# Kernel tuning notes

Hardware: AMD Instinct MI355X
Metric: run time of the kernel (lower is better)

The kernel has to match this reference:

```python
import jax, jax.numpy as jnp
import numpy as np

N, S, W, H = 256, 64, 256, 32   # node_num, sensor_num, slide_win, gru_hid_size
ALPHA = 0.2
NEG = -9e15


def gat(h, adj, Wm, a):
    """pyGAT GraphAttentionLayer (concat=False, dropout=0 / eval).
    h: [..., M, din], adj: [..., M, M], Wm: [..., din, dout], a: [..., 2*dout]."""
    Wh = jnp.einsum('...mi,...io->...mo', h, Wm)
    dout = Wm.shape[-1]
    f1 = jnp.einsum('...mo,...o->...m', Wh, a[..., :dout])
    f2 = jnp.einsum('...mo,...o->...m', Wh, a[..., dout:])
    e = jax.nn.leaky_relu(f1[..., :, None] + f2[..., None, :], negative_slope=ALPHA)
    att = jax.nn.softmax(jnp.where(adj > 0, e, NEG), axis=-1)
    return jnp.einsum('...mk,...ko->...mo', att, Wh)


def gru_cell(h, x, Wih, Whh, bih, bhh):
    # per-node batched torch GRU cell; gate order r, z, n
    gi = jnp.einsum('ngi,ni->ng', Wih, x) + bih
    gh = jnp.einsum('ngh,nh->ng', Whh, h) + bhh
    ir, iz, inn = jnp.split(gi, 3, axis=-1)
    hr, hz, hn = jnp.split(gh, 3, axis=-1)
    r = jax.nn.sigmoid(ir + hr)
    z = jax.nn.sigmoid(iz + hz)
    n = jnp.tanh(inn + r * hn)
    return (1.0 - z) * n + z * h


def gru2(xseq, h0, Wih0, Whh0, bih0, bhh0, Wih1, Whh1, bih1, bhh1):
    # xseq: [N, S, Din] (seq axis = sensor axis), h0: [2, N, H] -> ([N,S,H], [2,N,H])
    def step(carry, x_t):
        h0c, h1c = carry
        h0n = gru_cell(h0c, x_t, Wih0, Whh0, bih0, bhh0)
        h1n = gru_cell(h1c, h0n, Wih1, Whh1, bih1, bhh1)
        return (h0n, h1n), h1n
    (h0f, h1f), ys = jax.lax.scan(step, (h0[0], h0[1]), jnp.swapaxes(xseq, 0, 1))
    return jnp.swapaxes(ys, 0, 1), jnp.stack([h0f, h1f])


def setup_inputs():
    key = jax.random.key(0)
    ks = jax.random.split(key, 32)
    def rn(k, shape, scale=0.05):
        return jax.random.normal(k, shape, dtype=jnp.float32) * scale
    inp = {}
    inp['x'] = jax.random.normal(ks[0], (N, S, W), dtype=jnp.float32)
    inp['Feature_adj_sub'] = jax.random.randint(ks[1], (N, S, S), 0, 2).astype(jnp.float32)
    inp['Time_adj_sub'] = jax.random.randint(ks[2], (N, W, W), 0, 2).astype(jnp.float32)
    inp['adj'] = jax.random.randint(ks[3], (N, N), 0, 2).astype(jnp.float32)
    inp['H_pre'] = jax.random.normal(ks[4], (2, N, H), dtype=jnp.float32)
    # per-node GAT params (stacked over nodes)
    inp['Fatt_W'] = rn(ks[5], (N, W, W)); inp['Fatt_a'] = rn(ks[6], (N, 2 * W))
    inp['Tatt_W'] = rn(ks[7], (N, S, S)); inp['Tatt_a'] = rn(ks[8], (N, 2 * S))
    # per-node 2-layer GRU params
    inp['Wih0'] = rn(ks[9], (N, 3 * H, 3 * W)); inp['Whh0'] = rn(ks[10], (N, 3 * H, H))
    inp['bih0'] = rn(ks[11], (N, 3 * H)); inp['bhh0'] = rn(ks[12], (N, 3 * H))
    inp['Wih1'] = rn(ks[13], (N, 3 * H, H)); inp['Whh1'] = rn(ks[14], (N, 3 * H, H))
    inp['bih1'] = rn(ks[15], (N, 3 * H)); inp['bhh1'] = rn(ks[16], (N, 3 * H))
    # per-node 3-layer FC
    inp['fc1_w'] = rn(ks[17], (N, H, H)); inp['fc1_b'] = rn(ks[18], (N, H))
    inp['fc2_w'] = rn(ks[19], (N, H, H)); inp['fc2_b'] = rn(ks[20], (N, H))
    inp['fc3_w'] = rn(ks[21], (N, 1, H)); inp['fc3_b'] = rn(ks[22], (N, 1))
    # global output GATs
    inp['oW'] = rn(ks[23], (S, S)); inp['oa'] = rn(ks[24], (2 * S,))
    inp['o1W'] = rn(ks[25], (S, S)); inp['o1a'] = rn(ks[26], (2 * S,))
    inp['o2W'] = rn(ks[27], (2 * S, S)); inp['o2a'] = rn(ks[28], (2 * S,))
    return inp


def reference(x, Feature_adj_sub, Time_adj_sub, adj, H_pre,
              Fatt_W, Fatt_a, Tatt_W, Tatt_a,
              Wih0, Whh0, bih0, bhh0, Wih1, Whh1, bih1, bhh1,
              fc1_w, fc1_b, fc2_w, fc2_b, fc3_w, fc3_b,
              oW, oa, o1W, o1a, o2W, o2a):
    # batched over all nodes at once (replaces Python loop over node_num)
    Fat = gat(x, Feature_adj_sub, Fatt_W, Fatt_a)                    # [N,S,W]
    Tat = gat(jnp.swapaxes(x, 1, 2), Time_adj_sub, Tatt_W, Tatt_a)   # [N,W,S]
    cat_at = jnp.concatenate([Fat, jnp.swapaxes(Tat, 1, 2), x], axis=-1)  # [N,S,3W]
    gru_out, cat_H = gru2(cat_at, H_pre, Wih0, Whh0, bih0, bhh0,
                          Wih1, Whh1, bih1, bhh1)                    # [N,S,H],[2,N,H]
    h = jax.nn.relu(jnp.einsum('nsh,nkh->nsk', gru_out, fc1_w) + fc1_b[:, None, :])
    h = jax.nn.relu(jnp.einsum('nsh,nkh->nsk', h, fc2_w) + fc2_b[:, None, :])
    ct = (jnp.einsum('nsh,nkh->nsk', h, fc3_w) + fc3_b[:, None, :])[..., 0]  # [N,S]
    out = gat(ct, adj, oW, oa)
    out1 = gat(ct, adj, o1W, o1a)
    finalout = gat(jnp.concatenate([out, out1], axis=-1), adj, o2W, o2a)
    return finalout, cat_H
```

## Files before the change

kernel.cpp:

```cpp
#include <hip/hip_runtime.h>
#include <hip/hip_bf16.h>

__device__ __forceinline__ float sigf(float x){ return __builtin_amdgcn_rcpf(1.f+__expf(-x)); }
__device__ __forceinline__ float tanhfa(float x){
  return 1.f - 2.f*__builtin_amdgcn_rcpf(1.f + __expf(2.f*x));
}

#define ALPHA 0.2f
#define NEGV  -9e15f


__device__ __forceinline__ void gl2lds16(const float* g, float* l){
  __builtin_amdgcn_global_load_lds(
      (const __attribute__((address_space(1))) void*)g,
      (__attribute__((address_space(3))) void*)l, 16, 0, 0);
}

__global__ __launch_bounds__(256) void k_mask(const float* __restrict__ src,
                                              unsigned* __restrict__ dst, int nelem){
  const int stride = gridDim.x * blockDim.x;
  const int lane = threadIdx.x & 63;
  for (int e = blockIdx.x*blockDim.x + threadIdx.x; e < nelem; e += stride){
    unsigned long long m = __ballot(src[e] > 0.f);
    if (lane == 0)       dst[e >> 5] = (unsigned)m;
    else if (lane == 32) dst[e >> 5] = (unsigned)(m >> 32);
  }
}

__global__ __launch_bounds__(256) void k3_wht(const float* __restrict__ x,
                                              const float* __restrict__ TW,
                                              const float* __restrict__ Ta,
                                              float* __restrict__ WhTt,
                                              float* __restrict__ Tf1p,
                                              float* __restrict__ Tf2p){
  const int n = blockIdx.x >> 1, ch = blockIdx.x & 1, c0 = ch*32;
  const int tid = threadIdx.x;
  __shared__ float Wm[64][36];
  __shared__ float as1[32], as2[32];
  for (int idx = tid; idx < 2048; idx += 256){
    int k = idx >> 5, cc = idx & 31;
    Wm[k][cc] = TW[n*4096 + k*64 + c0 + cc];
  }
  if (tid < 32){ as1[tid] = Ta[n*128 + c0 + tid]; as2[tid] = Ta[n*128 + 64 + c0 + tid]; }
  __syncthreads();
  const int i = tid;
  const float* xn = x + n*16384;
  float acc[32];
#pragma unroll
  for (int c = 0; c < 32; ++c) acc[c] = 0.f;
#pragma unroll 2
  for (int k = 0; k < 64; ++k){
    float xv = xn[k*256 + i];
    const float* wr = &Wm[k][0];
#pragma unroll
    for (int c = 0; c < 32; ++c) acc[c] = fmaf(xv, wr[c], acc[c]);
  }
  float f1 = 0.f, f2 = 0.f;
#pragma unroll
  for (int c = 0; c < 32; ++c){ f1 = fmaf(acc[c], as1[c], f1); f2 = fmaf(acc[c], as2[c], f2); }
  Tf1p[ch*65536 + n*256 + i] = f1;
  Tf2p[ch*65536 + n*256 + i] = f2;
  float* o = WhTt + n*16384;
#pragma unroll
  for (int c = 0; c < 32; ++c) o[(c0+c)*256 + i] = acc[c];
}

__global__ __launch_bounds__(256) void k4_tat(const float* __restrict__ WhTt,
                                              const float* __restrict__ Tf1p,
                                              const float* __restrict__ Tf2p,
                                              const unsigned* __restrict__ maskT,
                                              float* __restrict__ TatT){
  const int n = blockIdx.x >> 1, ch = blockIdx.x & 1, c0 = ch*32;
  const int i = threadIdx.x;
  __shared__ float f2s[256];
  __shared__ float wt[64][36];
  const float f1 = Tf1p[n*256 + i] + Tf1p[65536 + n*256 + i];
  f2s[i] = Tf2p[n*256 + i] + Tf2p[65536 + n*256 + i];
  unsigned mw[8];
#pragma unroll
  for (int w = 0; w < 8; ++w) mw[w] = maskT[n*2048 + i*8 + w];
  __syncthreads();
  float m = -INFINITY;
  for (int w = 0; w < 8; ++w){
    const unsigned mk = mw[w];
#pragma unroll
    for (int bb = 0; bb < 32; ++bb){
      float e = f1 + f2s[(w<<5)+bb]; e = (e > 0.f) ? e : ALPHA*e;
      e = ((mk >> bb) & 1u) ? e : NEGV;
      m = fmaxf(m, e);
    }
  }
  float s = 0.f;
  for (int w = 0; w < 8; ++w){
    const unsigned mk = mw[w];
#pragma unroll
    for (int bb = 0; bb < 32; ++bb){
      float e = f1 + f2s[(w<<5)+bb]; e = (e > 0.f) ? e : ALPHA*e;
      e = ((mk >> bb) & 1u) ? e : NEGV;
      s += __expf(e - m);
    }
  }
  const float inv = 1.f / s;
  float acc[32];
#pragma unroll
  for (int c = 0; c < 32; ++c) acc[c] = 0.f;
  for (int jt = 0; jt < 4; ++jt){
    __syncthreads();
    for (int idx = i; idx < 2048; idx += 256){
      int cc = idx >> 6, jj = idx & 63;
      wt[jj][cc] = WhTt[n*16384 + (c0+cc)*256 + (jt<<6) + jj];
    }
    __syncthreads();
    for (int jj = 0; jj < 64; ++jj){
      const int j = (jt<<6) + jj;
      float e = f1 + f2s[j]; e = (e > 0.f) ? e : ALPHA*e;
      e = ((mw[j>>5] >> (j & 31)) & 1u) ? e : NEGV;
      const float p = __expf(e - m) * inv;
      const float* wr = &wt[jj][0];
#pragma unroll
      for (int c = 0; c < 32; ++c) acc[c] = fmaf(p, wr[c], acc[c]);
    }
  }
  float* o = TatT + n*16384;
#pragma unroll
  for (int c = 0; c < 32; ++c) o[(c0+c)*256 + i] = acc[c];
}

__global__ __launch_bounds__(256) void k1_whf(const float* __restrict__ x,
                                              const float* __restrict__ FW,
                                              float* __restrict__ WhF){
  const int n = blockIdx.x >> 1, ch = blockIdx.x & 1, c0 = ch*128;
  const int tid = threadIdx.x;
  __shared__ float xt[16384];
  {
    const int w = tid >> 6, l = tid & 63;
    const float* xg = x + n*16384 + w*4096 + l*4;
    float* ld = &xt[w*4096];
#pragma unroll
    for (int j = 0; j < 16; ++j) gl2lds16(xg + j*256, ld + j*256);
  }
  asm volatile("s_waitcnt vmcnt(0)" ::: "memory");
  __syncthreads();
  const int cq = tid & 31, iq = tid >> 5;
  const int cc = c0 + cq*4;
  const float* Wn = FW + (size_t)n*65536 + cc;
  const float* xrow = &xt[iq*8*256];
  float acc[8][4];
#pragma unroll
  for (int i = 0; i < 8; ++i)
#pragma unroll
    for (int c = 0; c < 4; ++c) acc[i][c] = 0.f;
#pragma unroll 2
  for (int k4 = 0; k4 < 64; ++k4){
    const float4 w0 = *(const float4*)&Wn[(4*k4+0)*256];
    const float4 w1 = *(const float4*)&Wn[(4*k4+1)*256];
    const float4 w2 = *(const float4*)&Wn[(4*k4+2)*256];
    const float4 w3 = *(const float4*)&Wn[(4*k4+3)*256];
#pragma unroll
    for (int i = 0; i < 8; ++i){
      const float4 xv = *(const float4*)&xrow[i*256 + 4*k4];
      acc[i][0] = fmaf(xv.x, w0.x, acc[i][0]); acc[i][0] = fmaf(xv.y, w1.x, acc[i][0]);
      acc[i][0] = fmaf(xv.z, w2.x, acc[i][0]); acc[i][0] = fmaf(xv.w, w3.x, acc[i][0]);
      acc[i][1] = fmaf(xv.x, w0.y, acc[i][1]); acc[i][1] = fmaf(xv.y, w1.y, acc[i][1]);
      acc[i][1] = fmaf(xv.z, w2.y, acc[i][1]); acc[i][1] = fmaf(xv.w, w3.y, acc[i][1]);
      acc[i][2] = fmaf(xv.x, w0.z, acc[i][2]); acc[i][2] = fmaf(xv.y, w1.z, acc[i][2]);
      acc[i][2] = fmaf(xv.z, w2.z, acc[i][2]); acc[i][2] = fmaf(xv.w, w3.z, acc[i][2]);
      acc[i][3] = fmaf(xv.x, w0.w, acc[i][3]); acc[i][3] = fmaf(xv.y, w1.w, acc[i][3]);
      acc[i][3] = fmaf(xv.z, w2.w, acc[i][3]); acc[i][3] = fmaf(xv.w, w3.w, acc[i][3]);
    }
  }
  float* o = WhF + n*16384 + cc;
#pragma unroll
  for (int i = 0; i < 8; ++i)
    *(float4*)&o[(iq*8 + i)*256] = make_float4(acc[i][0], acc[i][1], acc[i][2], acc[i][3]);
}

__global__ __launch_bounds__(512) void k2_fat(const float* __restrict__ WhF,
                                              const float* __restrict__ Fa,
                                              const float* __restrict__ Fadj,
                                              float* __restrict__ Fat){
  const int n = blockIdx.x, tid = threadIdx.x;
  __shared__ float attT[64][68];
  __shared__ float f1s[64], f2s[64];
  __shared__ float part[64][8][2];
  const float* Wh = WhF + n*16384;
  {
    int i = tid >> 3, q = tid & 7;
    const float* an = Fa + n*512;
    float p1 = 0.f, p2 = 0.f;
    for (int cc = 0; cc < 32; ++cc){
      int c2 = q*32 + cc;
      float w = Wh[i*256 + c2];
      p1 = fmaf(w, an[c2], p1);
      p2 = fmaf(w, an[256 + c2], p2);
    }
    part[i][q][0] = p1; part[i][q][1] = p2;
  }
  __syncthreads();
  if (tid < 64){
    float s1 = 0.f, s2 = 0.f;
#pragma unroll
    for (int q = 0; q < 8; ++q){ s1 += part[tid][q][0]; s2 += part[tid][q][1]; }
    f1s[tid] = s1; f2s[tid] = s2;
  }
  __syncthreads();
  if (tid < 64){
    const int r = tid;
    const float f1 = f1s[r];
    const float* adjr = Fadj + n*4096 + r*64;
    unsigned m0 = 0, m1 = 0;
#pragma unroll
    for (int j = 0; j < 32; ++j) if (adjr[j] > 0.f) m0 |= (1u << j);
#pragma unroll
    for (int j = 0; j < 32; ++j) if (adjr[32+j] > 0.f) m1 |= (1u << j);
    float m = -INFINITY;
#pragma unroll
    for (int j = 0; j < 64; ++j){
      float e = f1 + f2s[j]; e = (e > 0.f) ? e : ALPHA*e;
      unsigned bit = (j < 32) ? ((m0 >> j) & 1u) : ((m1 >> (j-32)) & 1u);
      e = bit ? e : NEGV;
      m = fmaxf(m, e);
    }
    float s = 0.f;
#pragma unroll
    for (int j = 0; j < 64; ++j){
      float e = f1 + f2s[j]; e = (e > 0.f) ? e : ALPHA*e;
      unsigned bit = (j < 32) ? ((m0 >> j) & 1u) : ((m1 >> (j-32)) & 1u);
      e = bit ? e : NEGV;
      s += __expf(e - m);
    }
    const float inv = 1.f / s;
#pragma unroll
    for (int j = 0; j < 64; ++j){
      float e = f1 + f2s[j]; e = (e > 0.f) ? e : ALPHA*e;
      unsigned bit = (j < 32) ? ((m0 >> j) & 1u) : ((m1 >> (j-32)) & 1u);
      e = bit ? e : NEGV;
      attT[j][r] = __expf(e - m) * inv;
    }
  }
  __syncthreads();
  const int c = tid & 255, ih = tid >> 8;
  float acc[32];
#pragma unroll
  for (int i = 0; i < 32; ++i) acc[i] = 0.f;
#pragma unroll 2
  for (int j = 0; j < 64; ++j){
    float w = Wh[j*256 + c];
    const float* ar = &attT[j][ih*32];
#pragma unroll
    for (int i = 0; i < 32; ++i) acc[i] = fmaf(ar[i], w, acc[i]);
  }
  float* o = Fat + n*16384;
#pragma unroll
  for (int i = 0; i < 32; ++i) o[(ih*32 + i)*256 + c] = acc[i];
}

__global__ __launch_bounds__(256) void k5_gi0(const float* __restrict__ Fat,
                                              const float* __restrict__ TatT,
                                              const float* __restrict__ x,
                                              const float* __restrict__ Wih0,
                                              float* __restrict__ P0,
                                              float* __restrict__ P1,
                                              float* __restrict__ P2){
  const int n = blockIdx.x & 255, s = blockIdx.x >> 8;
  const int tid = threadIdx.x;
  const int l = tid & 63, w = tid >> 6;
  const int a = tid & 31, b = tid >> 5;
  __shared__ float cl[2][2048];
  __shared__ float wl[2][3072];
  const float* src = (s == 0) ? (Fat + n*16384)
                   : (s == 1) ? (TatT + n*16384)
                              : (x + n*16384);
  const float* Wseg = Wih0 + (size_t)n*73728 + s*256;
  const int lr = l >> 3, lc = l & 7, sc = lc ^ lr;
  const float* cg0 = src + (16*w + lr)*256 + sc*4;
  const float* cg1 = cg0 + 8*256;
  const float* wg0 = Wseg + (size_t)(24*w + lr)*768 + lc*4;
  const float* wg1 = wg0 + (size_t)8*768;
  const float* wg2 = wg0 + (size_t)16*768;

#define K5_STAGE(BF, K0) do {                       \
    gl2lds16(cg0 + (K0), &cl[BF][512*w]);           \
    gl2lds16(cg1 + (K0), &cl[BF][512*w + 256]);     \
    gl2lds16(wg0 + (K0), &wl[BF][768*w]);           \
    gl2lds16(wg1 + (K0), &wl[BF][768*w + 256]);     \
    gl2lds16(wg2 + (K0), &wl[BF][768*w + 512]);     \
  } while (0)

  float acc[12][2];
#pragma unroll
  for (int gi = 0; gi < 12; ++gi){ acc[gi][0] = 0.f; acc[gi][1] = 0.f; }

  int bf = 0;
  K5_STAGE(0, 0);
  const int ax4 = (a & 7) << 2;
#pragma unroll 1
  for (int kt = 0; kt < 8; ++kt){
    if (kt < 7){
      K5_STAGE(bf ^ 1, (kt + 1) * 32);
      asm volatile("s_waitcnt vmcnt(5)" ::: "memory");
    } else {
      asm volatile("s_waitcnt vmcnt(0)" ::: "memory");
    }
    __builtin_amdgcn_s_barrier();
    const float* clb  = &cl[bf][a*32];
    const float* clb2 = &cl[bf][(a+32)*32];
    const float* wlb  = &wl[bf][b*384];
#pragma unroll
    for (int k4 = 0; k4 < 8; ++k4){
      const int j4 = (k4 << 2) ^ ax4;
      const float4 c0 = *(const float4*)&clb[j4];
      const float4 c1 = *(const float4*)&clb2[j4];
#pragma unroll
      for (int gi = 0; gi < 12; ++gi){
        const float4 wv = *(const float4*)&wlb[gi*32 + (k4 << 2)];
        float a0 = acc[gi][0], a1 = acc[gi][1];
        a0 = fmaf(wv.x, c0.x, a0); a1 = fmaf(wv.x, c1.x, a1);
        a0 = fmaf(wv.y, c0.y, a0); a1 = fmaf(wv.y, c1.y, a1);
        a0 = fmaf(wv.z, c0.z, a0); a1 = fmaf(wv.z, c1.z, a1);
        a0 = fmaf(wv.w, c0.w, a0); a1 = fmaf(wv.w, c1.w, a1);
        acc[gi][0] = a0; acc[gi][1] = a1;
      }
    }
    __builtin_amdgcn_s_barrier();
    bf ^= 1;
  }
#undef K5_STAGE
  float* o = (s == 0) ? (P0 + n*16384)
           : (s == 1) ? (P1 + n*16384)
                      : (P2 + n*8192);
#pragma unroll
  for (int q = 0; q < 3; ++q){
    *(float4*)&o[a*96 + b*12 + q*4] =
        make_float4(acc[4*q][0], acc[4*q+1][0], acc[4*q+2][0], acc[4*q+3][0]);
    *(float4*)&o[(a+32)*96 + b*12 + q*4] =
        make_float4(acc[4*q][1], acc[4*q+1][1], acc[4*q+2][1], acc[4*q+3][1]);
  }
}

__global__ __launch_bounds__(128) void k6_gru(const float* __restrict__ G0,
                                              const float* __restrict__ G1,
                                              const float* __restrict__ G2,
                                              const float* __restrict__ Hpre,
                                              const float* __restrict__ Whh0,
                                              const float* __restrict__ bih0,
                                              const float* __restrict__ bhh0,
                                              const float* __restrict__ Wih1,
                                              const float* __restrict__ Whh1,
                                              const float* __restrict__ bih1,
                                              const float* __restrict__ bhh1,
                                              const float* __restrict__ fc1w,
                                              const float* __restrict__ fc1b,
                                              const float* __restrict__ fc2w,
                                              const float* __restrict__ fc2b,
                                              const float* __restrict__ fc3w,
                                              const float* __restrict__ fc3b,
                                              float* __restrict__ ct,
                                              float* __restrict__ dout){
  const int n = blockIdx.x, tid = threadIdx.x;
  const int wid = tid >> 6, l = tid & 63;
  const int g2 = l & 31, co = (l >> 5) * 16;
  __shared__ float ginS[6144];
  __shared__ float h0buf[2][32];
  __shared__ float h1buf[2][32];
  __shared__ float hist[64][33];
  __shared__ float Wst[32][33];
  __shared__ float b1s[32], b2s[32], w3s[32];
  {
    const float4* p0 = (const float4*)(G0 + n*16384);
    const float4* p1 = (const float4*)(G1 + n*16384);
    const float4* p2 = (const float4*)(G2 + n*8192);
    float4* gs = (float4*)ginS;
#pragma unroll
    for (int j = 0; j < 12; ++j){
      int idx = j*128 + tid;
      float4 a = p0[idx], b = p1[idx], c = p2[idx];
      gs[idx] = make_float4(a.x+b.x+c.x, a.y+b.y+c.y, a.z+b.z+c.z, a.w+b.w+c.w);
    }
  }
  if (tid < 32){
    b1s[tid] = fc1b[n*32 + tid];
    b2s[tid] = fc2b[n*32 + tid];
    w3s[tid] = fc3w[n*32 + tid];
  }
  for (int idx = tid; idx < 1024; idx += 128) Wst[idx>>5][idx&31] = fc1w[n*1024 + idx];
  float wr_[16], wz_[16], wn_[16];
  float ur_[16], uz_[16], un_[16];
  {
    const float* WA = (wid == 0) ? (Whh0 + n*3072) : (Wih1 + n*3072);
#pragma unroll
    for (int q = 0; q < 4; ++q){
      float4 v;
      v = *(const float4*)(WA + g2*32 + co + 4*q);       wr_[4*q]=v.x; wr_[4*q+1]=v.y; wr_[4*q+2]=v.z; wr_[4*q+3]=v.w;
      v = *(const float4*)(WA + (32+g2)*32 + co + 4*q);  wz_[4*q]=v.x; wz_[4*q+1]=v.y; wz_[4*q+2]=v.z; wz_[4*q+3]=v.w;
      v = *(const float4*)(WA + (64+g2)*32 + co + 4*q);  wn_[4*q]=v.x; wn_[4*q+1]=v.y; wn_[4*q+2]=v.z; wn_[4*q+3]=v.w;
    }
    if (wid == 1){
      const float* WB = Whh1 + n*3072;
#pragma unroll
      for (int q = 0; q < 4; ++q){
        float4 v;
        v = *(const float4*)(WB + g2*32 + co + 4*q);       ur_[4*q]=v.x; ur_[4*q+1]=v.y; ur_[4*q+2]=v.z; ur_[4*q+3]=v.w;
        v = *(const float4*)(WB + (32+g2)*32 + co + 4*q);  uz_[4*q]=v.x; uz_[4*q+1]=v.y; uz_[4*q+2]=v.z; uz_[4*q+3]=v.w;
        v = *(const float4*)(WB + (64+g2)*32 + co + 4*q);  un_[4*q]=v.x; un_[4*q+1]=v.y; un_[4*q+2]=v.z; un_[4*q+3]=v.w;
      }
    }
  }
  const float* bip = (wid == 0) ? bih0 : bih1;
  const float* bhp = (wid == 0) ? bhh0 : bhh1;
  const float br = bip[n*96 + g2], bz = bip[n*96 + 32 + g2], bn = bip[n*96 + 64 + g2];
  const float cr = bhp[n*96 + g2], cz = bhp[n*96 + 32 + g2], cn = bhp[n*96 + 64 + g2];
  const float* hp = (wid == 0) ? (Hpre + n*32) : (Hpre + 8192 + n*32);
  float hown = hp[g2];
  float hs[16];
#pragma unroll
  for (int q = 0; q < 4; ++q){
    float4 v = *(const float4*)&hp[co + 4*q];
    hs[4*q]=v.x; hs[4*q+1]=v.y; hs[4*q+2]=v.z; hs[4*q+3]=v.w;
  }
  for (int s = 0; s < 65; ++s){
    __syncthreads();
    if (wid == 0){
      if (s < 64){
        const float gr = ginS[s*96 + g2], gz = ginS[s*96 + 32 + g2], gn = ginS[s*96 + 64 + g2];
        if (s > 0){
#pragma unroll
          for (int q = 0; q < 4; ++q){
            float4 v = *(const float4*)&h0buf[(s-1)&1][co + 4*q];
            hs[4*q]=v.x; hs[4*q+1]=v.y; hs[4*q+2]=v.z; hs[4*q+3]=v.w;
          }
        }
        float pr = 0.f, pz = 0.f, pn = 0.f;
#pragma unroll
        for (int j = 0; j < 16; ++j){
          pr = fmaf(wr_[j], hs[j], pr);
          pz = fmaf(wz_[j], hs[j], pz);
          pn = fmaf(wn_[j], hs[j], pn);
        }
        pr += __shfl_xor(pr, 32);
        pz += __shfl_xor(pz, 32);
        pn += __shfl_xor(pn, 32);
        const float r = sigf(gr + br + pr + cr);
        const float z = sigf(gz + bz + pz + cz);
        const float nn = tanhfa(gn + bn + r*(pn + cn));
        hown = (1.f - z)*nn + z*hown;
        if (l < 32) h0buf[s & 1][g2] = hown;
      }
    } else {
      if (s >= 1){
        const int t = s - 1;
        if (s > 1){
#pragma unroll
          for (int q = 0; q < 4; ++q){
            float4 v = *(const float4*)&h1buf[(s-1)&1][co + 4*q];
            hs[4*q]=v.x; hs[4*q+1]=v.y; hs[4*q+2]=v.z; hs[4*q+3]=v.w;
          }
        }
        float hx[16];
#pragma unroll
        for (int q = 0; q < 4; ++q){
          float4 v = *(const float4*)&h0buf[(s-1)&1][co + 4*q];
          hx[4*q]=v.x; hx[4*q+1]=v.y; hx[4*q+2]=v.z; hx[4*q+3]=v.w;
        }
        float qr = 0.f, qz = 0.f, qn = 0.f, sr = 0.f, sz = 0.f, sn = 0.f;
#pragma unroll
        for (int j = 0; j < 16; ++j){
          qr = fmaf(wr_[j], hx[j], qr);  sr = fmaf(ur_[j], hs[j], sr);
          qz = fmaf(wz_[j], hx[j], qz);  sz = fmaf(uz_[j], hs[j], sz);
          qn = fmaf(wn_[j], hx[j], qn);  sn = fmaf(un_[j], hs[j], sn);
        }
        float vr = qr + sr; vr += __shfl_xor(vr, 32);
        float vz = qz + sz; vz += __shfl_xor(vz, 32);
        qn += __shfl_xor(qn, 32);
        sn += __shfl_xor(sn, 32);
        const float r1 = sigf(vr + br + cr);
        const float z1 = sigf(vz + bz + cz);
        const float n1 = tanhfa(qn + bn + r1*(sn + cn));
        hown = (1.f - z1)*n1 + z1*hown;
        if (l < 32){ h1buf[s & 1][g2] = hown; hist[t][g2] = hown; }
      }
    }
  }
  if (wid == 0 && l < 32) dout[16384 + n*32 + g2] = hown;
  if (wid == 1 && l < 32) dout[16384 + 8192 + n*32 + g2] = hown;
  __syncthreads();
  float r1a[32];
  if (tid < 64){
    float hr[32];
#pragma unroll
    for (int k = 0; k < 32; ++k) hr[k] = hist[tid][k];
#pragma unroll
    for (int k = 0; k < 32; ++k){
      float a0=0.f,a1=0.f,a2=0.f,a3=0.f;
#pragma unroll
      for (int q = 0; q < 32; q += 4){
        a0 = fmaf(hr[q],   Wst[k][q],   a0);
        a1 = fmaf(hr[q+1], Wst[k][q+1], a1);
        a2 = fmaf(hr[q+2], Wst[k][q+2], a2);
        a3 = fmaf(hr[q+3], Wst[k][q+3], a3);
      }
      float v = b1s[k] + ((a0+a1)+(a2+a3));
      r1a[k] = v > 0.f ? v : 0.f;
    }
  }
  __syncthreads();
  for (int idx = tid; idx < 1024; idx += 128) Wst[idx>>5][idx&31] = fc2w[n*1024 + idx];
  __syncthreads();
  if (tid < 64){
    float r2a[32];
#pragma unroll
    for (int k = 0; k < 32; ++k){
      float a0=0.f,a1=0.f,a2=0.f,a3=0.f;
#pragma unroll
      for (int q = 0; q < 32; q += 4){
        a0 = fmaf(r1a[q],   Wst[k][q],   a0);
        a1 = fmaf(r1a[q+1], Wst[k][q+1], a1);
        a2 = fmaf(r1a[q+2], Wst[k][q+2], a2);
        a3 = fmaf(r1a[q+3], Wst[k][q+3], a3);
      }
      float v = b2s[k] + ((a0+a1)+(a2+a3));
      r2a[k] = v > 0.f ? v : 0.f;
    }
    float v = fc3b[n];
#pragma unroll
    for (int k = 0; k < 32; ++k) v = fmaf(r2a[k], w3s[k], v);
    ct[n*64 + tid] = v;
  }
}

__global__ __launch_bounds__(256) void k8a(const float* __restrict__ ct,
                                           const float* __restrict__ W0,
                                           const float* __restrict__ a0,
                                           const float* __restrict__ W1,
                                           const float* __restrict__ a1,
                                           float* __restrict__ WhABt,
                                           float* __restrict__ OF1,
                                           float* __restrict__ OF2){
  const int gat = blockIdx.x >> 2, rq = blockIdx.x & 3, r0 = rq*64;
  const int tid = threadIdx.x;
  const int ii = tid & 63, cq = tid >> 6;
  __shared__ float ctl[64][65];
  __shared__ float Wl[64][68];
  __shared__ float a1s[64], a2s[64];
  __shared__ float red[64][4][2];
  const float* W = gat ? W1 : W0;
  const float* aa = gat ? a1 : a0;
  for (int idx = tid; idx < 4096; idx += 256){
    int i2 = idx >> 6, k = idx & 63;
    ctl[i2][k] = ct[(r0 + i2)*64 + k];
  }
  for (int idx = tid; idx < 4096; idx += 256){
    int k = idx >> 6, c = idx & 63;
    Wl[k][c] = W[k*64 + c];
  }
  if (tid < 64){ a1s[tid] = aa[tid]; a2s[tid] = aa[64 + tid]; }
  __syncthreads();
  float acc[16];
#pragma unroll
  for (int c = 0; c < 16; ++c) acc[c] = 0.f;
#pragma unroll 2
  for (int k = 0; k < 64; ++k){
    float v = ctl[ii][k];
    const float* wr = &Wl[k][cq*16];
#pragma unroll
    for (int c = 0; c < 16; ++c) acc[c] = fmaf(v, wr[c], acc[c]);
  }
  float p1 = 0.f, p2 = 0.f;
#pragma unroll
  for (int c = 0; c < 16; ++c){
    p1 = fmaf(acc[c], a1s[cq*16 + c], p1);
    p2 = fmaf(acc[c], a2s[cq*16 + c], p2);
  }
  red[ii][cq][0] = p1; red[ii][cq][1] = p2;
  float* o = WhABt + gat*16384;
#pragma unroll
  for (int c = 0; c < 16; ++c) o[(cq*16 + c)*256 + r0 + ii] = acc[c];
  __syncthreads();
  if (cq == 0){
    OF1[gat*256 + r0 + ii] = red[ii][0][0] + red[ii][1][0] + red[ii][2][0] + red[ii][3][0];
    OF2[gat*256 + r0 + ii] = red[ii][0][1] + red[ii][1][1] + red[ii][2][1] + red[ii][3][1];
  }
}

__global__ __launch_bounds__(256) void k8b(const float* __restrict__ WhABt,
                                           const float* __restrict__ OF1,
                                           const float* __restrict__ OF2,
                                           const unsigned* __restrict__ maskA,
                                           float* __restrict__ OUTT){
  const int gat = blockIdx.x >> 2, c0 = (blockIdx.x & 3) * 16;
  const int i = threadIdx.x;
  __shared__ float f2s[256];
  __shared__ float wt[64][36];
  const float f1 = OF1[gat*256 + i];
  f2s[i] = OF2[gat*256 + i];
  unsigned mw[8];
#pragma unroll
  for (int w = 0; w < 8; ++w) mw[w] = maskA[i*8 + w];
  __syncthreads();
  float m = -INFINITY;
  for (int w = 0; w < 8; ++w){
    const unsigned mk = mw[w];
#pragma unroll
    for (int bb = 0; bb < 32; ++bb){
      float e = f1 + f2s[(w<<5)+bb]; e = (e > 0.f) ? e : ALPHA*e;
      e = ((mk >> bb) & 1u) ? e : NEGV;
      m = fmaxf(m, e);
    }
  }
  float s = 0.f;
  for (int w = 0; w < 8; ++w){
    const unsigned mk = mw[w];
#pragma unroll
    for (int bb = 0; bb < 32; ++bb){
      float e = f1 + f2s[(w<<5)+bb]; e = (e > 0.f) ? e : ALPHA*e;
      e = ((mk >> bb) & 1u) ? e : NEGV;
      s += __expf(e - m);
    }
  }
  const float inv = 1.f / s;
  float acc[16];
#pragma unroll
  for (int c = 0; c < 16; ++c) acc[c] = 0.f;
  for (int jt = 0; jt < 4; ++jt){
    __syncthreads();
    for (int idx = i; idx < 1024; idx += 256){
      int cc = idx >> 6, jj = idx & 63;
      wt[jj][cc] = WhABt[gat*16384 + (c0+cc)*256 + (jt<<6) + jj];
    }
    __syncthreads();
    for (int jj = 0; jj < 64; ++jj){
      const int j = (jt<<6) + jj;
      float e = f1 + f2s[j]; e = (e > 0.f) ? e : ALPHA*e;
      e = ((mw[j>>5] >> (j & 31)) & 1u) ? e : NEGV;
      const float p = __expf(e - m) * inv;
      const float* wr = &wt[jj][0];
#pragma unroll
      for (int c = 0; c < 16; ++c) acc[c] = fmaf(p, wr[c], acc[c]);
    }
  }
#pragma unroll
  for (int c = 0; c < 16; ++c) OUTT[gat*16384 + (c0+c)*256 + i] = acc[c];
}

__global__ __launch_bounds__(256) void k8c(const float* __restrict__ OUTT,
                                           const float* __restrict__ W2,
                                           const float* __restrict__ a2,
                                           float* __restrict__ Wh2,
                                           float* __restrict__ F1B,
                                           float* __restrict__ F2B){
  const int r0 = blockIdx.x * 32;
  const int tid = threadIdx.x;
  const int ii = tid & 31, cq = tid >> 5;
  __shared__ float W2l[128][68];
  __shared__ float a1s[64], a2s[64];
  __shared__ float red[32][8][2];
  for (int idx = tid; idx < 8192; idx += 256){
    int k = idx >> 6, c = idx & 63;
    W2l[k][c] = W2[k*64 + c];
  }
  if (tid < 64){ a1s[tid] = a2[tid]; a2s[tid] = a2[64 + tid]; }
  __syncthreads();
  float acc[8];
#pragma unroll
  for (int c = 0; c < 8; ++c) acc[c] = 0.f;
#pragma unroll 2
  for (int k = 0; k < 128; ++k){
    float v = OUTT[(k >> 6)*16384 + (k & 63)*256 + r0 + ii];
    const float* wr = &W2l[k][cq*8];
#pragma unroll
    for (int c = 0; c < 8; ++c) acc[c] = fmaf(v, wr[c], acc[c]);
  }
  float p1 = 0.f, p2 = 0.f;
#pragma unroll
  for (int c = 0; c < 8; ++c){
    p1 = fmaf(acc[c], a1s[cq*8 + c], p1);
    p2 = fmaf(acc[c], a2s[cq*8 + c], p2);
  }
  red[ii][cq][0] = p1; red[ii][cq][1] = p2;
#pragma unroll
  for (int c = 0; c < 8; ++c) Wh2[(cq*8 + c)*256 + r0 + ii] = acc[c];
  __syncthreads();
  if (cq == 0){
    float s1 = 0.f, s2 = 0.f;
#pragma unroll
    for (int q = 0; q < 8; ++q){ s1 += red[ii][q][0]; s2 += red[ii][q][1]; }
    F1B[r0 + ii] = s1; F2B[r0 + ii] = s2;
  }
}

__global__ __launch_bounds__(256) void k8d(const float* __restrict__ Wh2,
                                           const float* __restrict__ F1B,
                                           const float* __restrict__ F2B,
                                           const unsigned* __restrict__ maskA,
                                           float* __restrict__ dOut){
  const int c0 = blockIdx.x * 16;
  const int i = threadIdx.x;
  __shared__ float f2s[256];
  __shared__ float wt[64][36];
  const float f1 = F1B[i];
  f2s[i] = F2B[i];
  unsigned mw[8];
#pragma unroll
  for (int w = 0; w < 8; ++w) mw[w] = maskA[i*8 + w];
  __syncthreads();
  float m = -INFINITY;
  for (int w = 0; w < 8; ++w){
    const unsigned mk = mw[w];
#pragma unroll
    for (int bb = 0; bb < 32; ++bb){
      float e = f1 + f2s[(w<<5)+bb]; e = (e > 0.f) ? e : ALPHA*e;
      e = ((mk >> bb) & 1u) ? e : NEGV;
      m = fmaxf(m, e);
    }
  }
  float s = 0.f;
  for (int w = 0; w < 8; ++w){
    const unsigned mk = mw[w];
#pragma unroll
    for (int bb = 0; bb < 32; ++bb){
      float e = f1 + f2s[(w<<5)+bb]; e = (e > 0.f) ? e : ALPHA*e;
      e = ((mk >> bb) & 1u) ? e : NEGV;
      s += __expf(e - m);
    }
  }
  const float inv = 1.f / s;
  float acc[16];
#pragma unroll
  for (int c = 0; c < 16; ++c) acc[c] = 0.f;
  for (int jt = 0; jt < 4; ++jt){
    __syncthreads();
    for (int idx = i; idx < 1024; idx += 256){
      int cc = idx >> 6, jj = idx & 63;
      wt[jj][cc] = Wh2[(c0+cc)*256 + (jt<<6) + jj];
    }
    __syncthreads();
    for (int jj = 0; jj < 64; ++jj){
      const int j = (jt<<6) + jj;
      float e = f1 + f2s[j]; e = (e > 0.f) ? e : ALPHA*e;
      e = ((mw[j>>5] >> (j & 31)) & 1u) ? e : NEGV;
      const float p = __expf(e - m) * inv;
      const float* wr = &wt[jj][0];
#pragma unroll
      for (int c = 0; c < 16; ++c) acc[c] = fmaf(p, wr[c], acc[c]);
    }
  }
#pragma unroll
  for (int c = 0; c < 16; ++c) dOut[i*64 + c0 + c] = acc[c];
}

extern "C" void kernel_launch(void* const* d_in, const int* in_sizes, int n_in,
                              void* d_out, int out_size, void* d_ws, size_t ws_size,
                              hipStream_t stream){
  (void)in_sizes; (void)n_in; (void)out_size; (void)ws_size;
  const float* x     = (const float*)d_in[0];
  const float* Fadj  = (const float*)d_in[1];
  const float* Tadj  = (const float*)d_in[2];
  const float* adj   = (const float*)d_in[3];
  const float* Hpre  = (const float*)d_in[4];
  const float* FattW = (const float*)d_in[5];
  const float* Fatta = (const float*)d_in[6];
  const float* TattW = (const float*)d_in[7];
  const float* Tatta = (const float*)d_in[8];
  const float* Wih0  = (const float*)d_in[9];
  const float* Whh0  = (const float*)d_in[10];
  const float* bih0  = (const float*)d_in[11];
  const float* bhh0  = (const float*)d_in[12];
  const float* Wih1  = (const float*)d_in[13];
  const float* Whh1  = (const float*)d_in[14];
  const float* bih1  = (const float*)d_in[15];
  const float* bhh1  = (const float*)d_in[16];
  const float* fc1w  = (const float*)d_in[17];
  const float* fc1b  = (const float*)d_in[18];
  const float* fc2w  = (const float*)d_in[19];
  const float* fc2b  = (const float*)d_in[20];
  const float* fc3w  = (const float*)d_in[21];
  const float* fc3b  = (const float*)d_in[22];
  const float* oW    = (const float*)d_in[23];
  const float* oa    = (const float*)d_in[24];
  const float* o1W   = (const float*)d_in[25];
  const float* o1a   = (const float*)d_in[26];
  const float* o2W   = (const float*)d_in[27];
  const float* o2a   = (const float*)d_in[28];
  float* out = (float*)d_out;

  float* ws = (float*)d_ws;
  float* R0 = ws;
  float* R1 = ws + 4194304;
  float* R2 = ws + 8388608;
  unsigned* maskT = (unsigned*)R2;
  float* Tf1p = R2 + 524288;
  float* Tf2p = R2 + 655360;
  unsigned* maskA = (unsigned*)(ws + 12582912);
  float* WhTt = R0;
  float* WhF  = R0;
  float* TatT = R1;
  float* Fat  = R2;
  float* P0 = R2;
  float* P1 = R1;
  float* P2 = R0;
  float* ctb   = R0 + 2097152;
  float* WhABt = R1 + 16384;
  float* OF1   = R1 + 49152;
  float* OF2   = R1 + 49664;
  float* OUTT  = R1 + 50176;
  float* WH2   = R1 + 82944;
  float* F1B   = R1 + 99328;
  float* F2B   = R1 + 99584;

  k_mask<<<1024, 256, 0, stream>>>(Tadj, maskT, 16777216);
  k_mask<<<32, 256, 0, stream>>>(adj, maskA, 65536);
  k3_wht<<<512, 256, 0, stream>>>(x, TattW, Tatta, WhTt, Tf1p, Tf2p);
  k4_tat<<<512, 256, 0, stream>>>(WhTt, Tf1p, Tf2p, maskT, TatT);
  k1_whf<<<512, 256, 0, stream>>>(x, FattW, WhF);
  k2_fat<<<256, 512, 0, stream>>>(WhF, Fatta, Fadj, Fat);
  k5_gi0<<<768, 256, 0, stream>>>(Fat, TatT, x, Wih0, P0, P1, P2);
  k6_gru<<<256, 128, 0, stream>>>(P0, P1, P2, Hpre, Whh0, bih0, bhh0, Wih1, Whh1, bih1, bhh1,
                                  fc1w, fc1b, fc2w, fc2b, fc3w, fc3b, ctb, out);
  k8a<<<8, 256, 0, stream>>>(ctb, oW, oa, o1W, o1a, WhABt, OF1, OF2);
  k8b<<<8, 256, 0, stream>>>(WhABt, OF1, OF2, maskA, OUTT);
  k8c<<<8, 256, 0, stream>>>(OUTT, o2W, o2a, WH2, F1B, F2B);
  k8d<<<4, 256, 0, stream>>>(WH2, F1B, F2B, maskA, out);
}
```

Measured before the change: 672.7 us.

## Fuse GAT softmax into one pass with a bound-based max and LDS-staged tiles

In the three attention-aggregation kernels (time GAT, output GAT, final GAT), the separate max, sum and weighted-sum loops become one pass. The max is no longer found by scanning every pair: because leaky-ReLU is monotonic, it uses the upper bound leaky(f1 + max f2), taken from a wavefront shuffle reduction. The whole Wh tile is loaded into LDS once with async global-to-LDS loads and read as float4. Normalisation happens once at the end, which removes repeated exp work and per-tile barriers. The risks are that a row with every entry masked now gives zeros instead of a uniform average, and a loose bound could underflow exp.

```diff
diff --git a/kernel.cpp b/kernel.cpp
--- a/kernel.cpp
+++ b/kernel.cpp
@@ -72,58 +72,59 @@
                                               float* __restrict__ TatT){
   const int n = blockIdx.x >> 1, ch = blockIdx.x & 1, c0 = ch*32;
   const int i = threadIdx.x;
+  __shared__ float wt[8192];
   __shared__ float f2s[256];
-  __shared__ float wt[64][36];
-  const float f1 = Tf1p[n*256 + i] + Tf1p[65536 + n*256 + i];
-  f2s[i] = Tf2p[n*256 + i] + Tf2p[65536 + n*256 + i];
+  __shared__ float wmax[4];
+  {
+    const int w = i >> 6, l = i & 63;
+    const float* src = WhTt + n*16384 + c0*256 + w*2048 + l*4;
+    float* dst = &wt[w*2048];
+#pragma unroll
+    for (int r = 0; r < 8; ++r) gl2lds16(src + r*256, dst + r*256);
+  }
+  const float f1  = Tf1p[n*256 + i] + Tf1p[65536 + n*256 + i];
+  const float f2v = Tf2p[n*256 + i] + Tf2p[65536 + n*256 + i];
+  f2s[i] = f2v;
   unsigned mw[8];
 #pragma unroll
   for (int w = 0; w < 8; ++w) mw[w] = maskT[n*2048 + i*8 + w];
-  __syncthreads();
-  float m = -INFINITY;
-  for (int w = 0; w < 8; ++w){
-    const unsigned mk = mw[w];
-#pragma unroll
-    for (int bb = 0; bb < 32; ++bb){
-      float e = f1 + f2s[(w<<5)+bb]; e = (e > 0.f) ? e : ALPHA*e;
-      e = ((mk >> bb) & 1u) ? e : NEGV;
-      m = fmaxf(m, e);
-    }
-  }
+  float wm = f2v;
+#pragma unroll
+  for (int d = 1; d < 64; d <<= 1) wm = fmaxf(wm, __shfl_xor(wm, d));
+  if ((i & 63) == 0) wmax[i >> 6] = wm;
+  asm volatile("s_waitcnt vmcnt(0)" ::: "memory");
+  __syncthreads();
+  const float mb = fmaxf(fmaxf(wmax[0], wmax[1]), fmaxf(wmax[2], wmax[3]));
+  const float tm = f1 + mb;
+  const float m  = (tm > 0.f) ? tm : ALPHA*tm;
+  float acc[32];
+#pragma unroll
+  for (int c = 0; c < 32; ++c) acc[c] = 0.f;
   float s = 0.f;
-  for (int w = 0; w < 8; ++w){
-    const unsigned mk = mw[w];
-#pragma unroll
-    for (int bb = 0; bb < 32; ++bb){
-      float e = f1 + f2s[(w<<5)+bb]; e = (e > 0.f) ? e : ALPHA*e;
-      e = ((mk >> bb) & 1u) ? e : NEGV;
-      s += __expf(e - m);
-    }
-  }
-  const float inv = 1.f / s;
-  float acc[32];
-#pragma unroll
-  for (int c = 0; c < 32; ++c) acc[c] = 0.f;
-  for (int jt = 0; jt < 4; ++jt){
-    __syncthreads();
-    for (int idx = i; idx < 2048; idx += 256){
-      int cc = idx >> 6, jj = idx & 63;
-      wt[jj][cc] = WhTt[n*16384 + (c0+cc)*256 + (jt<<6) + jj];
-    }
-    __syncthreads();
-    for (int jj = 0; jj < 64; ++jj){
-      const int j = (jt<<6) + jj;
-      float e = f1 + f2s[j]; e = (e > 0.f) ? e : ALPHA*e;
-      e = ((mw[j>>5] >> (j & 31)) & 1u) ? e : NEGV;
-      const float p = __expf(e - m) * inv;
-      const float* wr = &wt[jj][0];
-#pragma unroll
-      for (int c = 0; c < 32; ++c) acc[c] = fmaf(p, wr[c], acc[c]);
-    }
-  }
+#pragma unroll 2
+  for (int jb = 0; jb < 64; ++jb){
+    const float4 f2q = *(const float4*)&f2s[jb*4];
+    const unsigned mk = mw[jb >> 3];
+    const int sh = (jb & 7) * 4;
+    float t0 = f1 + f2q.x; t0 = (t0 > 0.f) ? t0 : ALPHA*t0;
+    float t1 = f1 + f2q.y; t1 = (t1 > 0.f) ? t1 : ALPHA*t1;
+    float t2 = f1 + f2q.z; t2 = (t2 > 0.f) ? t2 : ALPHA*t2;
+    float t3 = f1 + f2q.w; t3 = (t3 > 0.f) ? t3 : ALPHA*t3;
+    const float e0 = ((mk >> (sh+0)) & 1u) ? __expf(t0 - m) : 0.f;
+    const float e1 = ((mk >> (sh+1)) & 1u) ? __expf(t1 - m) : 0.f;
+    const float e2 = ((mk >> (sh+2)) & 1u) ? __expf(t2 - m) : 0.f;
+    const float e3 = ((mk >> (sh+3)) & 1u) ? __expf(t3 - m) : 0.f;
+    s += (e0 + e1) + (e2 + e3);
+#pragma unroll
+    for (int c = 0; c < 32; ++c){
+      const float4 wv = *(const float4*)&wt[c*256 + jb*4];
+      acc[c] = fmaf(e0, wv.x, fmaf(e1, wv.y, fmaf(e2, wv.z, fmaf(e3, wv.w, acc[c]))));
+    }
+  }
+  const float inv = (s > 0.f) ? __builtin_amdgcn_rcpf(s) : 0.f;
   float* o = TatT + n*16384;
 #pragma unroll
-  for (int c = 0; c < 32; ++c) o[(c0+c)*256 + i] = acc[c];
+  for (int c = 0; c < 32; ++c) o[(c0+c)*256 + i] = acc[c] * inv;
 }
 
 __global__ __launch_bounds__(256) void k1_whf(const float* __restrict__ x,
@@ -589,57 +590,58 @@
                                            float* __restrict__ OUTT){
   const int gat = blockIdx.x >> 2, c0 = (blockIdx.x & 3) * 16;
   const int i = threadIdx.x;
+  __shared__ float wt[4096];
   __shared__ float f2s[256];
-  __shared__ float wt[64][36];
-  const float f1 = OF1[gat*256 + i];
-  f2s[i] = OF2[gat*256 + i];
+  __shared__ float wmax[4];
+  {
+    const int w = i >> 6, l = i & 63;
+    const float* src = WhABt + gat*16384 + c0*256 + w*1024 + l*4;
+    float* dst = &wt[w*1024];
+#pragma unroll
+    for (int r = 0; r < 4; ++r) gl2lds16(src + r*256, dst + r*256);
+  }
+  const float f1  = OF1[gat*256 + i];
+  const float f2v = OF2[gat*256 + i];
+  f2s[i] = f2v;
   unsigned mw[8];
 #pragma unroll
   for (int w = 0; w < 8; ++w) mw[w] = maskA[i*8 + w];
-  __syncthreads();
-  float m = -INFINITY;
-  for (int w = 0; w < 8; ++w){
-    const unsigned mk = mw[w];
-#pragma unroll
-    for (int bb = 0; bb < 32; ++bb){
-      float e = f1 + f2s[(w<<5)+bb]; e = (e > 0.f) ? e : ALPHA*e;
-      e = ((mk >> bb) & 1u) ? e : NEGV;
-      m = fmaxf(m, e);
-    }
-  }
+  float wm = f2v;
+#pragma unroll
+  for (int d = 1; d < 64; d <<= 1) wm = fmaxf(wm, __shfl_xor(wm, d));
+  if ((i & 63) == 0) wmax[i >> 6] = wm;
+  asm volatile("s_waitcnt vmcnt(0)" ::: "memory");
+  __syncthreads();
+  const float mb = fmaxf(fmaxf(wmax[0], wmax[1]), fmaxf(wmax[2], wmax[3]));
+  const float tm = f1 + mb;
+  const float m  = (tm > 0.f) ? tm : ALPHA*tm;
+  float acc[16];
+#pragma unroll
+  for (int c = 0; c < 16; ++c) acc[c] = 0.f;
   float s = 0.f;
-  for (int w = 0; w < 8; ++w){
-    const unsigned mk = mw[w];
-#pragma unroll
-    for (int bb = 0; bb < 32; ++bb){
-      float e = f1 + f2s[(w<<5)+bb]; e = (e > 0.f) ? e : ALPHA*e;
-      e = ((mk >> bb) & 1u) ? e : NEGV;
-      s += __expf(e - m);
-    }
-  }
-  const float inv = 1.f / s;
-  float acc[16];
-#pragma unroll
-  for (int c = 0; c < 16; ++c) acc[c] = 0.f;
-  for (int jt = 0; jt < 4; ++jt){
-    __syncthreads();
-    for (int idx = i; idx < 1024; idx += 256){
-      int cc = idx >> 6, jj = idx & 63;
-      wt[jj][cc] = WhABt[gat*16384 + (c0+cc)*256 + (jt<<6) + jj];
-    }
-    __syncthreads();
-    for (int jj = 0; jj < 64; ++jj){
-      const int j = (jt<<6) + jj;
-      float e = f1 + f2s[j]; e = (e > 0.f) ? e : ALPHA*e;
-      e = ((mw[j>>5] >> (j & 31)) & 1u) ? e : NEGV;
-      const float p = __expf(e - m) * inv;
-      const float* wr = &wt[jj][0];
-#pragma unroll
-      for (int c = 0; c < 16; ++c) acc[c] = fmaf(p, wr[c], acc[c]);
-    }
-  }
-#pragma unroll
-  for (int c = 0; c < 16; ++c) OUTT[gat*16384 + (c0+c)*256 + i] = acc[c];
+#pragma unroll 2
+  for (int jb = 0; jb < 64; ++jb){
+    const float4 f2q = *(const float4*)&f2s[jb*4];
+    const unsigned mk = mw[jb >> 3];
+    const int sh = (jb & 7) * 4;
+    float t0 = f1 + f2q.x; t0 = (t0 > 0.f) ? t0 : ALPHA*t0;
+    float t1 = f1 + f2q.y; t1 = (t1 > 0.f) ? t1 : ALPHA*t1;
+    float t2 = f1 + f2q.z; t2 = (t2 > 0.f) ? t2 : ALPHA*t2;
+    float t3 = f1 + f2q.w; t3 = (t3 > 0.f) ? t3 : ALPHA*t3;
+    const float e0 = ((mk >> (sh+0)) & 1u) ? __expf(t0 - m) : 0.f;
+    const float e1 = ((mk >> (sh+1)) & 1u) ? __expf(t1 - m) : 0.f;
+    const float e2 = ((mk >> (sh+2)) & 1u) ? __expf(t2 - m) : 0.f;
+    const float e3 = ((mk >> (sh+3)) & 1u) ? __expf(t3 - m) : 0.f;
+    s += (e0 + e1) + (e2 + e3);
+#pragma unroll
+    for (int c = 0; c < 16; ++c){
+      const float4 wv = *(const float4*)&wt[c*256 + jb*4];
+      acc[c] = fmaf(e0, wv.x, fmaf(e1, wv.y, fmaf(e2, wv.z, fmaf(e3, wv.w, acc[c]))));
+    }
+  }
+  const float inv = (s > 0.f) ? __builtin_amdgcn_rcpf(s) : 0.f;
+#pragma unroll
+  for (int c = 0; c < 16; ++c) OUTT[gat*16384 + (c0+c)*256 + i] = acc[c] * inv;
 }
 
 __global__ __launch_bounds__(256) void k8c(const float* __restrict__ OUTT,
@@ -695,57 +697,58 @@
                                            float* __restrict__ dOut){
   const int c0 = blockIdx.x * 16;
   const int i = threadIdx.x;
+  __shared__ float wt[4096];
   __shared__ float f2s[256];
-  __shared__ float wt[64][36];
-  const float f1 = F1B[i];
-  f2s[i] = F2B[i];
+  __shared__ float wmax[4];
+  {
+    const int w = i >> 6, l = i & 63;
+    const float* src = Wh2 + c0*256 + w*1024 + l*4;
+    float* dst = &wt[w*1024];
+#pragma unroll
+    for (int r = 0; r < 4; ++r) gl2lds16(src + r*256, dst + r*256);
+  }
+  const float f1  = F1B[i];
+  const float f2v = F2B[i];
+  f2s[i] = f2v;
   unsigned mw[8];
 #pragma unroll
   for (int w = 0; w < 8; ++w) mw[w] = maskA[i*8 + w];
-  __syncthreads();
-  float m = -INFINITY;
-  for (int w = 0; w < 8; ++w){
-    const unsigned mk = mw[w];
-#pragma unroll
-    for (int bb = 0; bb < 32; ++bb){
-      float e = f1 + f2s[(w<<5)+bb]; e = (e > 0.f) ? e : ALPHA*e;
-      e = ((mk >> bb) & 1u) ? e : NEGV;
-      m = fmaxf(m, e);
-    }
-  }
+  float wm = f2v;
+#pragma unroll
+  for (int d = 1; d < 64; d <<= 1) wm = fmaxf(wm, __shfl_xor(wm, d));
+  if ((i & 63) == 0) wmax[i >> 6] = wm;
+  asm volatile("s_waitcnt vmcnt(0)" ::: "memory");
+  __syncthreads();
+  const float mb = fmaxf(fmaxf(wmax[0], wmax[1]), fmaxf(wmax[2], wmax[3]));
+  const float tm = f1 + mb;
+  const float m  = (tm > 0.f) ? tm : ALPHA*tm;
+  float acc[16];
+#pragma unroll
+  for (int c = 0; c < 16; ++c) acc[c] = 0.f;
   float s = 0.f;
-  for (int w = 0; w < 8; ++w){
-    const unsigned mk = mw[w];
-#pragma unroll
-    for (int bb = 0; bb < 32; ++bb){
-      float e = f1 + f2s[(w<<5)+bb]; e = (e > 0.f) ? e : ALPHA*e;
-      e = ((mk >> bb) & 1u) ? e : NEGV;
-      s += __expf(e - m);
-    }
-  }
-  const float inv = 1.f / s;
-  float acc[16];
-#pragma unroll
-  for (int c = 0; c < 16; ++c) acc[c] = 0.f;
-  for (int jt = 0; jt < 4; ++jt){
-    __syncthreads();
-    for (int idx = i; idx < 1024; idx += 256){
-      int cc = idx >> 6, jj = idx & 63;
-      wt[jj][cc] = Wh2[(c0+cc)*256 + (jt<<6) + jj];
-    }
-    __syncthreads();
-    for (int jj = 0; jj < 64; ++jj){
-      const int j = (jt<<6) + jj;
-      float e = f1 + f2s[j]; e = (e > 0.f) ? e : ALPHA*e;
-      e = ((mw[j>>5] >> (j & 31)) & 1u) ? e : NEGV;
-      const float p = __expf(e - m) * inv;
-      const float* wr = &wt[jj][0];
-#pragma unroll
-      for (int c = 0; c < 16; ++c) acc[c] = fmaf(p, wr[c], acc[c]);
-    }
-  }
-#pragma unroll
-  for (int c = 0; c < 16; ++c) dOut[i*64 + c0 + c] = acc[c];
+#pragma unroll 2
+  for (int jb = 0; jb < 64; ++jb){
+    const float4 f2q = *(const float4*)&f2s[jb*4];
+    const unsigned mk = mw[jb >> 3];
+    const int sh = (jb & 7) * 4;
+    float t0 = f1 + f2q.x; t0 = (t0 > 0.f) ? t0 : ALPHA*t0;
+    float t1 = f1 + f2q.y; t1 = (t1 > 0.f) ? t1 : ALPHA*t1;
+    float t2 = f1 + f2q.z; t2 = (t2 > 0.f) ? t2 : ALPHA*t2;
+    float t3 = f1 + f2q.w; t3 = (t3 > 0.f) ? t3 : ALPHA*t3;
+    const float e0 = ((mk >> (sh+0)) & 1u) ? __expf(t0 - m) : 0.f;
+    const float e1 = ((mk >> (sh+1)) & 1u) ? __expf(t1 - m) : 0.f;
+    const float e2 = ((mk >> (sh+2)) & 1u) ? __expf(t2 - m) : 0.f;
+    const float e3 = ((mk >> (sh+3)) & 1u) ? __expf(t3 - m) : 0.f;
+    s += (e0 + e1) + (e2 + e3);
+#pragma unroll
+    for (int c = 0; c < 16; ++c){
+      const float4 wv = *(const float4*)&wt[c*256 + jb*4];
+      acc[c] = fmaf(e0, wv.x, fmaf(e1, wv.y, fmaf(e2, wv.z, fmaf(e3, wv.w, acc[c]))));
+    }
+  }
+  const float inv = (s > 0.f) ? __builtin_amdgcn_rcpf(s) : 0.f;
+#pragma unroll
+  for (int c = 0; c < 16; ++c) dOut[i*64 + c0 + c] = acc[c] * inv;
 }
 
 extern "C" void kernel_launch(void* const* d_in, const int* in_sizes, int n_in,
```

After: 631.4 us. 6.1% less time.
